# Kernel optimization log

Measured on AMD Instinct MI355X. Metric: run time of the kernel, lower is better.

The kernel has to match this reference:

```python
import jax, jax.numpy as jnp
import numpy as np

N = 33554432  # 32M elements, 128 MB fp32

def setup_inputs() -> dict:
    key = jax.random.key(0)
    inp = jax.random.uniform(key, (N,), dtype=jnp.float32)
    return {"inp": inp}

def reference(inp) -> jnp.ndarray:
    # Faithful to the original: exp(x) / sum(exp(inp)) with NO max-subtraction
    # (the torch module computes the unstabilized softmax).
    e = jnp.exp(inp)
    return e / jnp.sum(e)
```

## Files before the change

kernel.cpp:

```cpp
#include <hip/hip_runtime.h>


#define BLOCK 256
#define GRID 2048

__global__ __launch_bounds__(BLOCK) void softmax_reduce(
    const float* __restrict__ inp, float* __restrict__ sum_out, int n4) {
  const float4* __restrict__ in4 = (const float4*)inp;
  int tid = blockIdx.x * BLOCK + threadIdx.x;
  int stride = gridDim.x * BLOCK;

  float s = 0.0f;
  for (int i = tid; i < n4; i += stride) {
    float4 v = in4[i];
    s += __expf(v.x) + __expf(v.y) + __expf(v.z) + __expf(v.w);
  }

  #pragma unroll
  for (int off = 32; off > 0; off >>= 1)
    s += __shfl_down(s, off, 64);

  __shared__ float wsum[BLOCK / 64];
  int wave = threadIdx.x >> 6;
  int lane = threadIdx.x & 63;
  if (lane == 0) wsum[wave] = s;
  __syncthreads();
  if (threadIdx.x == 0) {
    float t = 0.0f;
    #pragma unroll
    for (int w = 0; w < BLOCK / 64; ++w) t += wsum[w];
    atomicAdd(sum_out, t);
  }
}

__global__ __launch_bounds__(BLOCK) void softmax_scale(
    const float* __restrict__ inp, float* __restrict__ out,
    const float* __restrict__ sum_ptr, int n4) {
  __shared__ float rinv_s;
  if (threadIdx.x == 0) rinv_s = 1.0f / (*sum_ptr);
  __syncthreads();
  float r = rinv_s;

  const float4* __restrict__ in4 = (const float4*)inp;
  float4* __restrict__ out4 = (float4*)out;
  int tid = blockIdx.x * BLOCK + threadIdx.x;
  int stride = gridDim.x * BLOCK;

  for (int i = tid; i < n4; i += stride) {
    float4 v = in4[i];
    float4 o;
    o.x = __expf(v.x) * r;
    o.y = __expf(v.y) * r;
    o.z = __expf(v.z) * r;
    o.w = __expf(v.w) * r;
    out4[i] = o;
  }
}

extern "C" void kernel_launch(void* const* d_in, const int* in_sizes, int n_in,
                              void* d_out, int out_size, void* d_ws, size_t ws_size,
                              hipStream_t stream) {
  const float* inp = (const float*)d_in[0];
  float* out = (float*)d_out;
  float* sum_ws = (float*)d_ws;
  int n = in_sizes[0];
  int n4 = n >> 2;

  hipMemsetAsync(sum_ws, 0, sizeof(float), stream);
  softmax_reduce<<<GRID, BLOCK, 0, stream>>>(inp, sum_ws, n4);
  softmax_scale<<<GRID, BLOCK, 0, stream>>>(inp, out, sum_ws, n4);
}
```

Baseline: 262.5 us.

## Replace atomic sum with per-block partials, unroll loops, use nontemporal stores

Drops the memset and the global atomicAdd. Each reduce block now writes its own partial sum, and every scale block re-reduces all 2048 partials itself. Both streaming loops are unrolled by two to keep more loads in flight, and the output uses nontemporal stores so it does not pollute the cache. The cost is that every scale block redundantly reads 2048 partials, and the reduction now assumes RGRID is a multiple of BLOCK.

```diff
diff --git a/kernel.cpp b/kernel.cpp
--- a/kernel.cpp
+++ b/kernel.cpp
@@ -2,58 +2,82 @@
 
 
 #define BLOCK 256
-#define GRID 2048
+#define RGRID 2048
+#define SGRID 2048
+
+typedef float vfloat4 __attribute__((ext_vector_type(4)));
 
 __global__ __launch_bounds__(BLOCK) void softmax_reduce(
-    const float* __restrict__ inp, float* __restrict__ sum_out, int n4) {
-  const float4* __restrict__ in4 = (const float4*)inp;
+    const float* __restrict__ inp, float* __restrict__ partials, int n4) {
+  const vfloat4* __restrict__ in4 = (const vfloat4*)inp;
   int tid = blockIdx.x * BLOCK + threadIdx.x;
   int stride = gridDim.x * BLOCK;
 
-  float s = 0.0f;
-  for (int i = tid; i < n4; i += stride) {
-    float4 v = in4[i];
-    s += __expf(v.x) + __expf(v.y) + __expf(v.z) + __expf(v.w);
+  float s0 = 0.0f, s1 = 0.0f;
+  int i = tid;
+  for (; i + stride < n4; i += 2 * stride) {
+    vfloat4 a = in4[i];
+    vfloat4 b = in4[i + stride];
+    s0 += __expf(a.x) + __expf(a.y) + __expf(a.z) + __expf(a.w);
+    s1 += __expf(b.x) + __expf(b.y) + __expf(b.z) + __expf(b.w);
   }
+  for (; i < n4; i += stride) {
+    vfloat4 a = in4[i];
+    s0 += __expf(a.x) + __expf(a.y) + __expf(a.z) + __expf(a.w);
+  }
+  float s = s0 + s1;
 
   #pragma unroll
   for (int off = 32; off > 0; off >>= 1)
     s += __shfl_down(s, off, 64);
 
   __shared__ float wsum[BLOCK / 64];
-  int wave = threadIdx.x >> 6;
-  int lane = threadIdx.x & 63;
-  if (lane == 0) wsum[wave] = s;
+  if ((threadIdx.x & 63) == 0) wsum[threadIdx.x >> 6] = s;
   __syncthreads();
-  if (threadIdx.x == 0) {
-    float t = 0.0f;
-    #pragma unroll
-    for (int w = 0; w < BLOCK / 64; ++w) t += wsum[w];
-    atomicAdd(sum_out, t);
-  }
+  if (threadIdx.x == 0)
+    partials[blockIdx.x] = wsum[0] + wsum[1] + wsum[2] + wsum[3];
 }
 
 __global__ __launch_bounds__(BLOCK) void softmax_scale(
     const float* __restrict__ inp, float* __restrict__ out,
-    const float* __restrict__ sum_ptr, int n4) {
-  __shared__ float rinv_s;
-  if (threadIdx.x == 0) rinv_s = 1.0f / (*sum_ptr);
+    const float* __restrict__ partials, int n4) {
+  float t = 0.0f;
+  #pragma unroll
+  for (int i = 0; i < RGRID / BLOCK; ++i)
+    t += partials[i * BLOCK + threadIdx.x];
+
+  #pragma unroll
+  for (int off = 32; off > 0; off >>= 1)
+    t += __shfl_down(t, off, 64);
+
+  __shared__ float wsum[BLOCK / 64];
+  if ((threadIdx.x & 63) == 0) wsum[threadIdx.x >> 6] = t;
   __syncthreads();
-  float r = rinv_s;
+  float r = 1.0f / (wsum[0] + wsum[1] + wsum[2] + wsum[3]);
 
-  const float4* __restrict__ in4 = (const float4*)inp;
-  float4* __restrict__ out4 = (float4*)out;
+  const vfloat4* __restrict__ in4 = (const vfloat4*)inp;
+  vfloat4* __restrict__ out4 = (vfloat4*)out;
   int tid = blockIdx.x * BLOCK + threadIdx.x;
   int stride = gridDim.x * BLOCK;
 
-  for (int i = tid; i < n4; i += stride) {
-    float4 v = in4[i];
-    float4 o;
-    o.x = __expf(v.x) * r;
-    o.y = __expf(v.y) * r;
-    o.z = __expf(v.z) * r;
-    o.w = __expf(v.w) * r;
-    out4[i] = o;
+  int i = tid;
+  for (; i + stride < n4; i += 2 * stride) {
+    vfloat4 a = in4[i];
+    vfloat4 b = in4[i + stride];
+    vfloat4 oa, ob;
+    oa.x = __expf(a.x) * r; oa.y = __expf(a.y) * r;
+    oa.z = __expf(a.z) * r; oa.w = __expf(a.w) * r;
+    ob.x = __expf(b.x) * r; ob.y = __expf(b.y) * r;
+    ob.z = __expf(b.z) * r; ob.w = __expf(b.w) * r;
+    __builtin_nontemporal_store(oa, &out4[i]);
+    __builtin_nontemporal_store(ob, &out4[i + stride]);
+  }
+  for (; i < n4; i += stride) {
+    vfloat4 a = in4[i];
+    vfloat4 oa;
+    oa.x = __expf(a.x) * r; oa.y = __expf(a.y) * r;
+    oa.z = __expf(a.z) * r; oa.w = __expf(a.w) * r;
+    __builtin_nontemporal_store(oa, &out4[i]);
   }
 }
 
@@ -62,11 +86,10 @@
                               hipStream_t stream) {
   const float* inp = (const float*)d_in[0];
   float* out = (float*)d_out;
-  float* sum_ws = (float*)d_ws;
+  float* partials = (float*)d_ws;
   int n = in_sizes[0];
   int n4 = n >> 2;
 
-  hipMemsetAsync(sum_ws, 0, sizeof(float), stream);
-  softmax_reduce<<<GRID, BLOCK, 0, stream>>>(inp, sum_ws, n4);
-  softmax_scale<<<GRID, BLOCK, 0, stream>>>(inp, out, sum_ws, n4);
+  softmax_reduce<<<RGRID, BLOCK, 0, stream>>>(inp, partials, n4);
+  softmax_scale<<<SGRID, BLOCK, 0, stream>>>(inp, out, partials, n4);
 }
```

Measured after the change: 247.6 us. -5.7%, faster.
